# Kernel optimization log

Measured on AMD Instinct MI355X. Metric: run time of the kernel, lower is better.

The kernel has to match this reference:

```python
import jax, jax.numpy as jnp
import numpy as np

N, M, FEAT, POS, D, MSG, NCLS = 64, 32, 256, 6, 262, 128, 7


def setup_inputs() -> dict:
    key = jax.random.key(0)
    ks = jax.random.split(key, 12)
    s = 0.05
    p = lambda k, shape: jax.random.normal(k, shape, jnp.float32) * s
    return {
        "nodes_feature": jax.random.normal(ks[0], (N, M, FEAT), jnp.float32),
        "pos": jax.random.normal(ks[1], (N, M, POS), jnp.float32),
        "num_rec": jax.random.randint(ks[2], (N,), 1, M + 1),
        "link_w1": p(ks[3], (D, 2 * D)),
        "link_b1": jnp.zeros((D,), jnp.float32),
        "link_w2": p(ks[4], (D,)),
        "link_b2": jnp.zeros((), jnp.float32),
        "msg_w": p(ks[5], (MSG, D)),
        "msg_b": jnp.zeros((MSG,), jnp.float32),
        "gru_w_ih": p(ks[6], (3 * D, MSG)),
        "gru_w_hh": p(ks[7], (3 * D, D)),
        "gru_b_ih": jnp.zeros((3 * D,), jnp.float32),
        "gru_b_hh": jnp.zeros((3 * D,), jnp.float32),
        "ro_w1": p(ks[8], (MSG, D)),
        "ro_b1": jnp.zeros((MSG,), jnp.float32),
        "ro_w2": p(ks[9], (NCLS, MSG)),
        "ro_b2": jnp.zeros((NCLS,), jnp.float32),
    }


def reference(nodes_feature, pos, num_rec, link_w1, link_b1, link_w2, link_b2,
              msg_w, msg_b, gru_w_ih, gru_w_hh, gru_b_ih, gru_b_hh,
              ro_w1, ro_b1, ro_w2, ro_b2):
    # node_feat = [resnet_feat, pos]  -> (N, M, 262)
    nf = jnp.concatenate([nodes_feature, pos], axis=-1)
    n, m, d = nf.shape
    valid = jnp.arange(m)[None, :] < num_rec[:, None]          # (N, M)
    pair = valid[:, :, None] & valid[:, None, :]               # (N, M, M)

    # edge_feat[b,:,i,j] = concat(nf[b,i], nf[b,j]); zero for invalid pairs
    ef = jnp.concatenate([
        jnp.broadcast_to(nf[:, :, None, :], (n, m, m, d)),
        jnp.broadcast_to(nf[:, None, :, :], (n, m, m, d)),
    ], axis=-1) * pair[..., None].astype(nf.dtype)             # (N, M, M, 2D)

    # 1x1 convs == per-pair MLP
    hlink = jax.nn.relu(jnp.einsum('bnwc,dc->bnwd', ef, link_w1) + link_b1)
    attmat = jax.nn.sigmoid(jnp.einsum('bnwd,d->bnw', hlink, link_w2) + link_b2)

    # messages are only summed over valid sender nodes w
    att_m = attmat * valid[:, None, :].astype(attmat.dtype)    # (N, M, M)

    def gru_step(x, h):
        # PyTorch GRU cell: gates order (r, z, n)
        gx = x @ gru_w_ih.T + gru_b_ih
        gh = h @ gru_w_hh.T + gru_b_hh
        xr, xz, xn = jnp.split(gx, 3, axis=-1)
        hr, hz, hn = jnp.split(gh, 3, axis=-1)
        r = jax.nn.sigmoid(xr + hr)
        z = jax.nn.sigmoid(xz + hz)
        c = jnp.tanh(xn + r * hn)
        return (1.0 - z) * c + z * h

    vmask = valid[..., None].astype(nf.dtype)
    h_state = nf                                               # pass 0 input state
    for _ in range(2):                                         # two message-passing rounds
        msg = h_state @ msg_w.T + msg_b                        # (N, M, 128)
        m_v = jnp.einsum('bnw,bwk->bnk', att_m, msg)           # attention-weighted sum
        h_state = gru_step(m_v, h_state) * vmask               # invalid nodes stay zero

    pred = (jax.nn.relu(h_state @ ro_w1.T + ro_b1) @ ro_w2.T + ro_b2) * vmask
    return pred, attmat
```

## Files before the change

### kernel.cpp

```cpp
#include <hip/hip_runtime.h>
#include <math.h>

#define N_G   64
#define M_N   32
#define FEAT  256
#define POSD  6
#define D     262
#define MSG   128
#define NCLS  7

#define KA_S  424
#define KHW   288
#define KFULL 416
#define PSTR  320

#define S_PROJ (528*288)
#define S_MSG  (128*288)
#define S_RZ   (544*416)
#define S_XN   (272*128)
#define S_HN   (272*288)
#define S_RO   (128*288)
#define S_RO2  (16*128)

#define O_WPROJ 0u
#define O_WMSG  76032u
#define O_WRZ   94464u
#define O_WXN   207616u
#define O_WHN   225024u
#define O_WRO   264192u
#define O_WRO2  282624u
#define O_GB    283648u

typedef __attribute__((ext_vector_type(8))) short short8;
typedef __attribute__((ext_vector_type(4))) short short4v;
typedef __attribute__((ext_vector_type(4))) float floatx4;

#define MFMA __builtin_amdgcn_mfma_f32_16x16x32_bf16

__device__ __forceinline__ short f2bf(float f) {
    union { float f; unsigned u; } v; v.f = f;
    unsigned r = v.u + 0x7FFF + ((v.u >> 16) & 1);
    return (short)(r >> 16);
}
__device__ __forceinline__ float bf2f(short s) {
    union { float f; unsigned u; } v;
    v.u = ((unsigned)(unsigned short)s) << 16;
    return v.f;
}
__device__ __forceinline__ float sigf(float x) { return 1.f / (1.f + expf(-x)); }

__global__ void prep_kernel(const float* __restrict__ w1, const float* __restrict__ msg_w,
                            const float* __restrict__ w_ih, const float* __restrict__ w_hh,
                            const float* __restrict__ ro_w1, const float* __restrict__ ro_w2,
                            const float* __restrict__ b_ih, const float* __restrict__ b_hh,
                            float* __restrict__ ws)
{
    short* wproj = (short*)(ws + O_WPROJ);
    short* wmsg  = (short*)(ws + O_WMSG);
    short* wrz   = (short*)(ws + O_WRZ);
    short* wxn   = (short*)(ws + O_WXN);
    short* whn   = (short*)(ws + O_WHN);
    short* wro   = (short*)(ws + O_WRO);
    short* wro2  = (short*)(ws + O_WRO2);
    float* gb    = ws + O_GB;
    const int TOT_S = S_PROJ + S_MSG + S_RZ + S_XN + S_HN + S_RO + S_RO2;
    const int TOTAL = TOT_S + 1088;
    for (int i = blockIdx.x * blockDim.x + threadIdx.x; i < TOTAL;
         i += gridDim.x * blockDim.x) {
        int idx = i;
        if (idx < S_PROJ) {
            int n = idx / 288, k = idx % 288;
            float v = 0.f;
            if (k < D && n < 524)
                v = (n < D) ? w1[n * 524 + k] : w1[(n - D) * 524 + D + k];
            wproj[idx] = f2bf(v);
            continue;
        }
        idx -= S_PROJ;
        if (idx < S_MSG) {
            int n = idx / 288, k = idx % 288;
            wmsg[idx] = f2bf(k < D ? msg_w[n * D + k] : 0.f);
            continue;
        }
        idx -= S_MSG;
        if (idx < S_RZ) {
            int g = idx / 416, k = idx % 416;
            int gi = (g < 272) ? 0 : 1;
            int d = g - gi * 272;
            float v = 0.f;
            if (d < D) {
                int row = gi * D + d;
                if (k < 128)            v = w_ih[row * MSG + k];
                else if (k < 128 + D)   v = w_hh[row * D + (k - 128)];
            }
            wrz[idx] = f2bf(v);
            continue;
        }
        idx -= S_RZ;
        if (idx < S_XN) {
            int d = idx / 128, k = idx % 128;
            wxn[idx] = f2bf(d < D ? w_ih[(2 * D + d) * MSG + k] : 0.f);
            continue;
        }
        idx -= S_XN;
        if (idx < S_HN) {
            int d = idx / 288, k = idx % 288;
            whn[idx] = f2bf((d < D && k < D) ? w_hh[(2 * D + d) * D + k] : 0.f);
            continue;
        }
        idx -= S_HN;
        if (idx < S_RO) {
            int n = idx / 288, k = idx % 288;
            wro[idx] = f2bf(k < D ? ro_w1[n * D + k] : 0.f);
            continue;
        }
        idx -= S_RO;
        if (idx < S_RO2) {
            int n = idx / 128, k = idx % 128;
            wro2[idx] = f2bf(n < NCLS ? ro_w2[n * MSG + k] : 0.f);
            continue;
        }
        idx -= S_RO2;
        {
            int seg = idx / 272, d = idx % 272;
            float v = 0.f;
            if (d < D) {
                if (seg == 0)      v = b_ih[d] + b_hh[d];
                else if (seg == 1) v = b_ih[D + d] + b_hh[D + d];
                else if (seg == 2) v = b_ih[2 * D + d];
                else               v = b_hh[2 * D + d];
            }
            gb[idx] = v;
        }
    }
}

__global__ __launch_bounds__(512, 2) void fused_kernel(
    const float* __restrict__ nodes, const float* __restrict__ pos,
    const int* __restrict__ nrec_g,
    const float* __restrict__ b1g, const float* __restrict__ w2g,
    const float* __restrict__ b2g, const float* __restrict__ msg_bg,
    const float* __restrict__ ro_b1g, const float* __restrict__ ro_b2g,
    const float* __restrict__ ws,
    float* __restrict__ att_out, float* __restrict__ pred)
{
    const short* Wproj = (const short*)(ws + O_WPROJ);
    const short* Wmsg  = (const short*)(ws + O_WMSG);
    const short* Wrz   = (const short*)(ws + O_WRZ);
    const short* Wxn   = (const short*)(ws + O_WXN);
    const short* Whn   = (const short*)(ws + O_WHN);
    const short* Wro   = (const short*)(ws + O_WRO);
    const short* Wro2  = (const short*)(ws + O_WRO2);
    const float* gb    = ws + O_GB;

    __shared__ __align__(16) short bufA[32 * KA_S];
    __shared__ __align__(16) short bufB[32 * KA_S];
    __shared__ __align__(16) short paL[32 * PSTR];
    __shared__ __align__(16) short pbL[32 * PSTR];
    __shared__ __align__(16) short attL[32 * 40];
    __shared__ __align__(16) short msgT[128 * 40];
    __shared__ __align__(16) short hidL[32 * 136];
    __shared__ __align__(16) float b1L[PSTR], w2L[PSTR];

    const int b = blockIdx.x;
    const int tid = threadIdx.x;
    const int wave = tid >> 6, lane = tid & 63;
    const int quad = lane >> 4, lrow = lane & 15;
    const int nr = nrec_g[b];

    for (int idx = tid; idx < 32 * 64; idx += 512) {
        int w = idx >> 6, c4 = idx & 63;
        floatx4 v = *(const floatx4*)(nodes + ((size_t)(b * 32 + w)) * FEAT + c4 * 4);
        short4v s; s[0] = f2bf(v[0]); s[1] = f2bf(v[1]); s[2] = f2bf(v[2]); s[3] = f2bf(v[3]);
        *(short4v*)(bufA + w * KA_S + 128 + c4 * 4) = s;
    }
    for (int idx = tid; idx < 32 * POSD; idx += 512) {
        int w = idx / POSD, c = idx % POSD;
        bufA[w * KA_S + 128 + FEAT + c] = f2bf(pos[((size_t)(b * 32 + w)) * POSD + c]);
    }
    for (int idx = tid; idx < 32 * 34; idx += 512) {
        int w = idx / 34, c = idx % 34;
        bufA[w * KA_S + 390 + c] = 0;
        bufB[w * KA_S + 390 + c] = 0;
    }
    for (int idx = tid; idx < 32 * (PSTR - D); idx += 512) {
        int w = idx / (PSTR - D), c = idx % (PSTR - D);
        paL[w * PSTR + D + c] = 0;
        pbL[w * PSTR + D + c] = 0;
    }
    for (int d = tid; d < PSTR; d += 512) {
        b1L[d] = (d < D) ? b1g[d] : 0.f;
        w2L[d] = (d < D) ? w2g[d] : 0.f;
    }
    __syncthreads();

    for (int s = wave; s < 33; s += 8) {
        floatx4 acc0 = {}, acc1 = {};
        const short* bw = Wproj + (s * 16 + lrow) * KHW + quad * 8;
        const short* ap = bufA + lrow * KA_S + 128 + quad * 8;
        for (int kk = 0; kk < 9; ++kk) {
            short8 a0 = *(const short8*)(ap + kk * 32);
            short8 a1 = *(const short8*)(ap + 16 * KA_S + kk * 32);
            short8 bv = *(const short8*)(bw + kk * 32);
            acc0 = MFMA(a0, bv, acc0, 0, 0, 0);
            acc1 = MFMA(a1, bv, acc1, 0, 0, 0);
        }
        int col = s * 16 + lrow;
#pragma unroll
        for (int rr = 0; rr < 4; ++rr) {
            int r0 = quad * 4 + rr;
            if (col < D) {
                paL[r0 * PSTR + col] = f2bf(acc0[rr]);
                paL[(r0 + 16) * PSTR + col] = f2bf(acc1[rr]);
            } else if (col < 2 * D) {
                pbL[r0 * PSTR + (col - D)] = f2bf(acc0[rr]);
                pbL[(r0 + 16) * PSTR + (col - D)] = f2bf(acc1[rr]);
            }
        }
    }
    __syncthreads();

    {
        const int grp = tid >> 4;
        const int c16 = tid & 15;
        const float b2v = b2g[0];
        float pav[5][4], b1v[5][4], w2v[5][4];
#pragma unroll
        for (int k = 0; k < 5; ++k) {
            int dbase = c16 * 4 + 64 * k;
            short4v p = *(const short4v*)(paL + grp * PSTR + dbase);
            floatx4 bb = *(const floatx4*)(b1L + dbase);
            floatx4 ww = *(const floatx4*)(w2L + dbase);
#pragma unroll
            for (int e = 0; e < 4; ++e) {
                pav[k][e] = bf2f(p[e]); b1v[k][e] = bb[e]; w2v[k][e] = ww[e];
            }
        }
        float p0 = 0.f;
#pragma unroll
        for (int k = 0; k < 5; ++k)
#pragma unroll
            for (int e = 0; e < 4; ++e)
                p0 += fmaxf(b1v[k][e], 0.f) * w2v[k][e];
        p0 += __shfl_down(p0, 8, 16); p0 += __shfl_down(p0, 4, 16);
        p0 += __shfl_down(p0, 2, 16); p0 += __shfl_down(p0, 1, 16);
        float c0 = sigf(p0 + b2v);
        const bool vi = grp < nr;
        for (int j = 0; j < 32; ++j) {
            float a;
            if (j < nr && vi) {
                const short* pb = pbL + j * PSTR + c16 * 4;
                float s = 0.f;
#pragma unroll
                for (int k = 0; k < 5; ++k) {
                    short4v q = *(const short4v*)(pb + 64 * k);
#pragma unroll
                    for (int e = 0; e < 4; ++e) {
                        float v = pav[k][e] + bf2f(q[e]) + b1v[k][e];
                        s += fmaxf(v, 0.f) * w2v[k][e];
                    }
                }
                s += __shfl_down(s, 8, 16); s += __shfl_down(s, 4, 16);
                s += __shfl_down(s, 2, 16); s += __shfl_down(s, 1, 16);
                a = sigf(s + b2v);
            } else {
                a = c0;
            }
            if (c16 == 0) {
                att_out[((size_t)(b * 32 + grp)) * 32 + j] = a;
                attL[grp * 40 + j] = f2bf((j < nr) ? a : 0.f);
            }
        }
    }
    __syncthreads();

    for (int rnd = 0; rnd < 2; ++rnd) {
        short* src = rnd ? bufB : bufA;
        short* dst = rnd ? bufA : bufB;

        {
            int s = wave;
            floatx4 acc0 = {}, acc1 = {};
            const short* bw = Wmsg + (s * 16 + lrow) * KHW + quad * 8;
            const short* ap = src + lrow * KA_S + 128 + quad * 8;
            for (int kk = 0; kk < 9; ++kk) {
                short8 a0 = *(const short8*)(ap + kk * 32);
                short8 a1 = *(const short8*)(ap + 16 * KA_S + kk * 32);
                short8 bv = *(const short8*)(bw + kk * 32);
                acc0 = MFMA(a0, bv, acc0, 0, 0, 0);
                acc1 = MFMA(a1, bv, acc1, 0, 0, 0);
            }
            int col = s * 16 + lrow;
            float bias = msg_bg[col];
#pragma unroll
            for (int rr = 0; rr < 4; ++rr) {
                msgT[col * 40 + quad * 4 + rr] = f2bf(acc0[rr] + bias);
                msgT[col * 40 + 16 + quad * 4 + rr] = f2bf(acc1[rr] + bias);
            }
        }
        __syncthreads();

        {
            int mi = wave & 1, ng = wave >> 1;
            short8 afrag = *(const short8*)(attL + (mi * 16 + lrow) * 40 + quad * 8);
            floatx4 acc0 = {}, acc1 = {};
            short8 bf0 = *(const short8*)(msgT + (ng * 32 + lrow) * 40 + quad * 8);
            short8 bf1 = *(const short8*)(msgT + (ng * 32 + 16 + lrow) * 40 + quad * 8);
            acc0 = MFMA(afrag, bf0, acc0, 0, 0, 0);
            acc1 = MFMA(afrag, bf1, acc1, 0, 0, 0);
#pragma unroll
            for (int rr = 0; rr < 4; ++rr) {
                int m = mi * 16 + quad * 4 + rr;
                src[m * KA_S + ng * 32 + lrow] = f2bf(acc0[rr]);
                src[m * KA_S + ng * 32 + 16 + lrow] = f2bf(acc1[rr]);
            }
        }
        __syncthreads();

        for (int s = wave; s < 17; s += 8) {
            floatx4 aR0 = {}, aR1 = {}, aZ0 = {}, aZ1 = {};
            floatx4 aN0 = {}, aN1 = {}, aH0 = {}, aH1 = {};
            const short* ap  = src + lrow * KA_S + quad * 8;
            const short* bpr = Wrz + (s * 16 + lrow) * KFULL + quad * 8;
            const short* bpz = Wrz + (272 + s * 16 + lrow) * KFULL + quad * 8;
            const short* bpx = Wxn + (s * 16 + lrow) * 128 + quad * 8;
            const short* bph = Whn + (s * 16 + lrow) * KHW + quad * 8;
            for (int kk = 0; kk < 13; ++kk) {
                short8 a0 = *(const short8*)(ap + kk * 32);
                short8 a1 = *(const short8*)(ap + 16 * KA_S + kk * 32);
                short8 br = *(const short8*)(bpr + kk * 32);
                short8 bz = *(const short8*)(bpz + kk * 32);
                aR0 = MFMA(a0, br, aR0, 0, 0, 0);
                aR1 = MFMA(a1, br, aR1, 0, 0, 0);
                aZ0 = MFMA(a0, bz, aZ0, 0, 0, 0);
                aZ1 = MFMA(a1, bz, aZ1, 0, 0, 0);
                if (kk < 4) {
                    short8 bx = *(const short8*)(bpx + kk * 32);
                    aN0 = MFMA(a0, bx, aN0, 0, 0, 0);
                    aN1 = MFMA(a1, bx, aN1, 0, 0, 0);
                } else {
                    short8 bh = *(const short8*)(bph + (kk - 4) * 32);
                    aH0 = MFMA(a0, bh, aH0, 0, 0, 0);
                    aH1 = MFMA(a1, bh, aH1, 0, 0, 0);
                }
            }
            int d = s * 16 + lrow;
            if (d < D) {
                float bgr = gb[d], bgz = gb[272 + d];
                float bxv = gb[544 + d], bhv = gb[816 + d];
#pragma unroll
                for (int i = 0; i < 2; ++i) {
                    floatx4 vR = i ? aR1 : aR0, vZ = i ? aZ1 : aZ0;
                    floatx4 vN = i ? aN1 : aN0, vH = i ? aH1 : aH0;
#pragma unroll
                    for (int rr = 0; rr < 4; ++rr) {
                        int m = i * 16 + quad * 4 + rr;
                        float rg = sigf(vR[rr] + bgr);
                        float zg = sigf(vZ[rr] + bgz);
                        float cg = tanhf(vN[rr] + bxv + rg * (vH[rr] + bhv));
                        float hold = bf2f(src[m * KA_S + 128 + d]);
                        float hv = (1.f - zg) * cg + zg * hold;
                        if (m >= nr) hv = 0.f;
                        dst[m * KA_S + 128 + d] = f2bf(hv);
                    }
                }
            }
        }
        __syncthreads();
    }

    {
        int s = wave;
        floatx4 acc0 = {}, acc1 = {};
        const short* bw = Wro + (s * 16 + lrow) * KHW + quad * 8;
        const short* ap = bufA + lrow * KA_S + 128 + quad * 8;
        for (int kk = 0; kk < 9; ++kk) {
            short8 a0 = *(const short8*)(ap + kk * 32);
            short8 a1 = *(const short8*)(ap + 16 * KA_S + kk * 32);
            short8 bv = *(const short8*)(bw + kk * 32);
            acc0 = MFMA(a0, bv, acc0, 0, 0, 0);
            acc1 = MFMA(a1, bv, acc1, 0, 0, 0);
        }
        int col = s * 16 + lrow;
        float bias = ro_b1g[col];
#pragma unroll
        for (int rr = 0; rr < 4; ++rr) {
            hidL[(quad * 4 + rr) * 136 + col] = f2bf(fmaxf(acc0[rr] + bias, 0.f));
            hidL[(16 + quad * 4 + rr) * 136 + col] = f2bf(fmaxf(acc1[rr] + bias, 0.f));
        }
    }
    __syncthreads();

    if (wave == 0) {
        floatx4 acc0 = {}, acc1 = {};
        const short* ap = hidL + lrow * 136 + quad * 8;
        const short* bw = Wro2 + lrow * 128 + quad * 8;
        for (int kk = 0; kk < 4; ++kk) {
            short8 a0 = *(const short8*)(ap + kk * 32);
            short8 a1 = *(const short8*)(ap + 16 * 136 + kk * 32);
            short8 bv = *(const short8*)(bw + kk * 32);
            acc0 = MFMA(a0, bv, acc0, 0, 0, 0);
            acc1 = MFMA(a1, bv, acc1, 0, 0, 0);
        }
        int q = lrow;
        if (q < NCLS) {
            float bias = ro_b2g[q];
#pragma unroll
            for (int i = 0; i < 2; ++i) {
#pragma unroll
                for (int rr = 0; rr < 4; ++rr) {
                    int m = i * 16 + quad * 4 + rr;
                    float v = (i ? acc1[rr] : acc0[rr]) + bias;
                    if (m >= nr) v = 0.f;
                    pred[((size_t)(b * 32 + m)) * NCLS + q] = v;
                }
            }
        }
    }
}

extern "C" void kernel_launch(void* const* d_in, const int* in_sizes, int n_in,
                              void* d_out, int out_size, void* d_ws, size_t ws_size,
                              hipStream_t stream)
{
    const float* nodes = (const float*)d_in[0];
    const float* pos   = (const float*)d_in[1];
    const int*   nrec  = (const int*)d_in[2];
    const float* w1    = (const float*)d_in[3];
    const float* b1    = (const float*)d_in[4];
    const float* w2    = (const float*)d_in[5];
    const float* b2    = (const float*)d_in[6];
    const float* msg_w = (const float*)d_in[7];
    const float* msg_b = (const float*)d_in[8];
    const float* w_ih  = (const float*)d_in[9];
    const float* w_hh  = (const float*)d_in[10];
    const float* b_ih  = (const float*)d_in[11];
    const float* b_hh  = (const float*)d_in[12];
    const float* ro_w1 = (const float*)d_in[13];
    const float* ro_b1 = (const float*)d_in[14];
    const float* ro_w2 = (const float*)d_in[15];
    const float* ro_b2 = (const float*)d_in[16];
    float* ws   = (float*)d_ws;
    float* pred = (float*)d_out;
    float* attout = pred + (size_t)N_G * M_N * NCLS;

    prep_kernel<<<256, 256, 0, stream>>>(w1, msg_w, w_ih, w_hh, ro_w1, ro_w2,
                                         b_ih, b_hh, ws);
    fused_kernel<<<N_G, 512, 0, stream>>>(nodes, pos, nrec, b1, w2, b2, msg_b,
                                          ro_b1, ro_b2, ws, attout, pred);
}
```

Before: 160.4 us.

## Double block size to 1024 threads and repartition work across 16 waves

Raises the per-graph block from 512 to 1024 threads and splits each stage's work across 16 waves instead of 8: message, aggregation and readout GEMMs now give each wave a single 16-row tile, and the pairwise attention loop splits the j range between two thread groups. The link bias b1 is folded into the projected pa values once, and the inner attention loop now uses 8-wide bf16 loads over a padded stride of 384. With only 64 blocks on the GPU, the goal is more parallelism per graph to cut latency. The cost is fewer registers per thread under the 1024-thread bound and more barrier participants. Some loops, such as the GRU stage with 17 slabs, leave waves idle.

```diff
diff --git a/kernel.cpp b/kernel.cpp
--- a/kernel.cpp
+++ b/kernel.cpp
@@ -9,10 +9,11 @@
 #define MSG   128
 #define NCLS  7
 
+#define NT    1024
 #define KA_S  424
 #define KHW   288
 #define KFULL 416
-#define PSTR  320
+#define PSTR  384
 
 #define S_PROJ (528*288)
 #define S_MSG  (128*288)
@@ -135,7 +136,7 @@
     }
 }
 
-__global__ __launch_bounds__(512, 2) void fused_kernel(
+__global__ __launch_bounds__(NT, 4) void fused_kernel(
     const float* __restrict__ nodes, const float* __restrict__ pos,
     const int* __restrict__ nrec_g,
     const float* __restrict__ b1g, const float* __restrict__ w2g,
@@ -168,33 +169,33 @@
     const int quad = lane >> 4, lrow = lane & 15;
     const int nr = nrec_g[b];
 
-    for (int idx = tid; idx < 32 * 64; idx += 512) {
+    for (int idx = tid; idx < 32 * 64; idx += NT) {
         int w = idx >> 6, c4 = idx & 63;
         floatx4 v = *(const floatx4*)(nodes + ((size_t)(b * 32 + w)) * FEAT + c4 * 4);
         short4v s; s[0] = f2bf(v[0]); s[1] = f2bf(v[1]); s[2] = f2bf(v[2]); s[3] = f2bf(v[3]);
         *(short4v*)(bufA + w * KA_S + 128 + c4 * 4) = s;
     }
-    for (int idx = tid; idx < 32 * POSD; idx += 512) {
+    for (int idx = tid; idx < 32 * POSD; idx += NT) {
         int w = idx / POSD, c = idx % POSD;
         bufA[w * KA_S + 128 + FEAT + c] = f2bf(pos[((size_t)(b * 32 + w)) * POSD + c]);
     }
-    for (int idx = tid; idx < 32 * 34; idx += 512) {
+    for (int idx = tid; idx < 32 * 34; idx += NT) {
         int w = idx / 34, c = idx % 34;
         bufA[w * KA_S + 390 + c] = 0;
         bufB[w * KA_S + 390 + c] = 0;
     }
-    for (int idx = tid; idx < 32 * (PSTR - D); idx += 512) {
+    for (int idx = tid; idx < 32 * (PSTR - D); idx += NT) {
         int w = idx / (PSTR - D), c = idx % (PSTR - D);
         paL[w * PSTR + D + c] = 0;
         pbL[w * PSTR + D + c] = 0;
     }
-    for (int d = tid; d < PSTR; d += 512) {
+    for (int d = tid; d < PSTR; d += NT) {
         b1L[d] = (d < D) ? b1g[d] : 0.f;
         w2L[d] = (d < D) ? w2g[d] : 0.f;
     }
     __syncthreads();
 
-    for (int s = wave; s < 33; s += 8) {
+    for (int s = wave; s < 33; s += 16) {
         floatx4 acc0 = {}, acc1 = {};
         const short* bw = Wproj + (s * 16 + lrow) * KHW + quad * 8;
         const short* ap = bufA + lrow * KA_S + 128 + quad * 8;
@@ -210,8 +211,9 @@
         for (int rr = 0; rr < 4; ++rr) {
             int r0 = quad * 4 + rr;
             if (col < D) {
-                paL[r0 * PSTR + col] = f2bf(acc0[rr]);
-                paL[(r0 + 16) * PSTR + col] = f2bf(acc1[rr]);
+                float bb = b1L[col];
+                paL[r0 * PSTR + col] = f2bf(acc0[rr] + bb);
+                paL[(r0 + 16) * PSTR + col] = f2bf(acc1[rr] + bb);
             } else if (col < 2 * D) {
                 pbL[r0 * PSTR + (col - D)] = f2bf(acc0[rr]);
                 pbL[(r0 + 16) * PSTR + (col - D)] = f2bf(acc1[rr]);
@@ -222,43 +224,51 @@
 
     {
         const int grp = tid >> 4;
+        const int i = grp >> 1;
+        const int jb = (grp & 1) * 16;
         const int c16 = tid & 15;
         const float b2v = b2g[0];
-        float pav[5][4], b1v[5][4], w2v[5][4];
-#pragma unroll
-        for (int k = 0; k < 5; ++k) {
-            int dbase = c16 * 4 + 64 * k;
-            short4v p = *(const short4v*)(paL + grp * PSTR + dbase);
-            floatx4 bb = *(const floatx4*)(b1L + dbase);
-            floatx4 ww = *(const floatx4*)(w2L + dbase);
+        float pav[3][8], w2v[3][8];
+#pragma unroll
+        for (int k = 0; k < 3; ++k) {
+            int dbase = c16 * 8 + 128 * k;
+            short8 p = *(const short8*)(paL + i * PSTR + dbase);
+            floatx4 wa = *(const floatx4*)(w2L + dbase);
+            floatx4 wb = *(const floatx4*)(w2L + dbase + 4);
 #pragma unroll
             for (int e = 0; e < 4; ++e) {
-                pav[k][e] = bf2f(p[e]); b1v[k][e] = bb[e]; w2v[k][e] = ww[e];
+                pav[k][e] = bf2f(p[e]); pav[k][4 + e] = bf2f(p[4 + e]);
+                w2v[k][e] = wa[e]; w2v[k][4 + e] = wb[e];
             }
         }
         float p0 = 0.f;
 #pragma unroll
-        for (int k = 0; k < 5; ++k)
-#pragma unroll
-            for (int e = 0; e < 4; ++e)
-                p0 += fmaxf(b1v[k][e], 0.f) * w2v[k][e];
+        for (int k = 0; k < 3; ++k) {
+            int dbase = c16 * 8 + 128 * k;
+            floatx4 ba = *(const floatx4*)(b1L + dbase);
+            floatx4 bb = *(const floatx4*)(b1L + dbase + 4);
+#pragma unroll
+            for (int e = 0; e < 4; ++e) {
+                p0 += fmaxf(ba[e], 0.f) * w2v[k][e];
+                p0 += fmaxf(bb[e], 0.f) * w2v[k][4 + e];
+            }
+        }
         p0 += __shfl_down(p0, 8, 16); p0 += __shfl_down(p0, 4, 16);
         p0 += __shfl_down(p0, 2, 16); p0 += __shfl_down(p0, 1, 16);
         float c0 = sigf(p0 + b2v);
-        const bool vi = grp < nr;
-        for (int j = 0; j < 32; ++j) {
+        const bool vi = i < nr;
+        for (int jj = 0; jj < 16; ++jj) {
+            int j = jb + jj;
             float a;
-            if (j < nr && vi) {
-                const short* pb = pbL + j * PSTR + c16 * 4;
+            if (vi && j < nr) {
+                const short* pb = pbL + j * PSTR + c16 * 8;
                 float s = 0.f;
 #pragma unroll
-                for (int k = 0; k < 5; ++k) {
-                    short4v q = *(const short4v*)(pb + 64 * k);
-#pragma unroll
-                    for (int e = 0; e < 4; ++e) {
-                        float v = pav[k][e] + bf2f(q[e]) + b1v[k][e];
-                        s += fmaxf(v, 0.f) * w2v[k][e];
-                    }
+                for (int k = 0; k < 3; ++k) {
+                    short8 q = *(const short8*)(pb + 128 * k);
+#pragma unroll
+                    for (int e = 0; e < 8; ++e)
+                        s += fmaxf(pav[k][e] + bf2f(q[e]), 0.f) * w2v[k][e];
                 }
                 s += __shfl_down(s, 8, 16); s += __shfl_down(s, 4, 16);
                 s += __shfl_down(s, 2, 16); s += __shfl_down(s, 1, 16);
@@ -267,8 +277,8 @@
                 a = c0;
             }
             if (c16 == 0) {
-                att_out[((size_t)(b * 32 + grp)) * 32 + j] = a;
-                attL[grp * 40 + j] = f2bf((j < nr) ? a : 0.f);
+                att_out[((size_t)(b * 32 + i)) * 32 + j] = a;
+                attL[i * 40 + j] = f2bf((j < nr) ? a : 0.f);
             }
         }
     }
@@ -279,45 +289,38 @@
         short* dst = rnd ? bufA : bufB;
 
         {
-            int s = wave;
-            floatx4 acc0 = {}, acc1 = {};
+            int s = wave >> 1, mi = wave & 1;
+            floatx4 acc = {};
             const short* bw = Wmsg + (s * 16 + lrow) * KHW + quad * 8;
-            const short* ap = src + lrow * KA_S + 128 + quad * 8;
+            const short* ap = src + (mi * 16 + lrow) * KA_S + 128 + quad * 8;
             for (int kk = 0; kk < 9; ++kk) {
                 short8 a0 = *(const short8*)(ap + kk * 32);
-                short8 a1 = *(const short8*)(ap + 16 * KA_S + kk * 32);
                 short8 bv = *(const short8*)(bw + kk * 32);
-                acc0 = MFMA(a0, bv, acc0, 0, 0, 0);
-                acc1 = MFMA(a1, bv, acc1, 0, 0, 0);
+                acc = MFMA(a0, bv, acc, 0, 0, 0);
             }
             int col = s * 16 + lrow;
             float bias = msg_bg[col];
 #pragma unroll
-            for (int rr = 0; rr < 4; ++rr) {
-                msgT[col * 40 + quad * 4 + rr] = f2bf(acc0[rr] + bias);
-                msgT[col * 40 + 16 + quad * 4 + rr] = f2bf(acc1[rr] + bias);
-            }
+            for (int rr = 0; rr < 4; ++rr)
+                msgT[col * 40 + mi * 16 + quad * 4 + rr] = f2bf(acc[rr] + bias);
         }
         __syncthreads();
 
         {
             int mi = wave & 1, ng = wave >> 1;
             short8 afrag = *(const short8*)(attL + (mi * 16 + lrow) * 40 + quad * 8);
-            floatx4 acc0 = {}, acc1 = {};
-            short8 bf0 = *(const short8*)(msgT + (ng * 32 + lrow) * 40 + quad * 8);
-            short8 bf1 = *(const short8*)(msgT + (ng * 32 + 16 + lrow) * 40 + quad * 8);
-            acc0 = MFMA(afrag, bf0, acc0, 0, 0, 0);
-            acc1 = MFMA(afrag, bf1, acc1, 0, 0, 0);
+            short8 bfrag = *(const short8*)(msgT + (ng * 16 + lrow) * 40 + quad * 8);
+            floatx4 acc = {};
+            acc = MFMA(afrag, bfrag, acc, 0, 0, 0);
 #pragma unroll
             for (int rr = 0; rr < 4; ++rr) {
                 int m = mi * 16 + quad * 4 + rr;
-                src[m * KA_S + ng * 32 + lrow] = f2bf(acc0[rr]);
-                src[m * KA_S + ng * 32 + 16 + lrow] = f2bf(acc1[rr]);
+                src[m * KA_S + ng * 16 + lrow] = f2bf(acc[rr]);
             }
         }
         __syncthreads();
 
-        for (int s = wave; s < 17; s += 8) {
+        for (int s = wave; s < 17; s += 16) {
             floatx4 aR0 = {}, aR1 = {}, aZ0 = {}, aZ1 = {};
             floatx4 aN0 = {}, aN1 = {}, aH0 = {}, aH1 = {};
             const short* ap  = src + lrow * KA_S + quad * 8;
@@ -370,24 +373,20 @@
     }
 
     {
-        int s = wave;
-        floatx4 acc0 = {}, acc1 = {};
+        int s = wave >> 1, mi = wave & 1;
+        floatx4 acc = {};
         const short* bw = Wro + (s * 16 + lrow) * KHW + quad * 8;
-        const short* ap = bufA + lrow * KA_S + 128 + quad * 8;
+        const short* ap = bufA + (mi * 16 + lrow) * KA_S + 128 + quad * 8;
         for (int kk = 0; kk < 9; ++kk) {
             short8 a0 = *(const short8*)(ap + kk * 32);
-            short8 a1 = *(const short8*)(ap + 16 * KA_S + kk * 32);
             short8 bv = *(const short8*)(bw + kk * 32);
-            acc0 = MFMA(a0, bv, acc0, 0, 0, 0);
-            acc1 = MFMA(a1, bv, acc1, 0, 0, 0);
+            acc = MFMA(a0, bv, acc, 0, 0, 0);
         }
         int col = s * 16 + lrow;
         float bias = ro_b1g[col];
 #pragma unroll
-        for (int rr = 0; rr < 4; ++rr) {
-            hidL[(quad * 4 + rr) * 136 + col] = f2bf(fmaxf(acc0[rr] + bias, 0.f));
-            hidL[(16 + quad * 4 + rr) * 136 + col] = f2bf(fmaxf(acc1[rr] + bias, 0.f));
-        }
+        for (int rr = 0; rr < 4; ++rr)
+            hidL[(mi * 16 + quad * 4 + rr) * 136 + col] = f2bf(fmaxf(acc[rr] + bias, 0.f));
     }
     __syncthreads();
 
@@ -446,6 +445,6 @@
 
     prep_kernel<<<256, 256, 0, stream>>>(w1, msg_w, w_ih, w_hh, ro_w1, ro_w2,
                                          b_ih, b_hh, ws);
-    fused_kernel<<<N_G, 512, 0, stream>>>(nodes, pos, nrec, b1, w2, b2, msg_b,
-                                          ro_b1, ro_b2, ws, attout, pred);
+    fused_kernel<<<N_G, NT, 0, stream>>>(nodes, pos, nrec, b1, w2, b2, msg_b,
+                                         ro_b1, ro_b2, ws, attout, pred);
 }
```

Measured after the change: 195.2 us. 1.22x slower.

## Restructure attention pair loop, fold link bias into projection, use fast transcendentals

Applied to the files above, without the earlier changes.

The pairwise attention stage is remapped so each lane computes one (i,j) pair for two rows directly over the full feature dimension. This replaces the earlier scheme of 16-lane groups looping serially over j with shuffle reductions. The link bias b1 is folded into the projected pa values, and the constant attention value for invalid pairs is now computed once in the prep kernel. Sigmoid and tanh switch to hardware exp2/rcp intrinsics, and the shared-memory row stride shrinks to 266. The risks are LDS bank conflicts from the odd stride and slightly lower precision in the activations.

```diff
diff --git a/kernel.cpp b/kernel.cpp
--- a/kernel.cpp
+++ b/kernel.cpp
@@ -12,7 +12,7 @@
 #define KA_S  424
 #define KHW   288
 #define KFULL 416
-#define PSTR  320
+#define PSTR  266
 
 #define S_PROJ (528*288)
 #define S_MSG  (128*288)
@@ -47,12 +47,21 @@
     v.u = ((unsigned)(unsigned short)s) << 16;
     return v.f;
 }
-__device__ __forceinline__ float sigf(float x) { return 1.f / (1.f + expf(-x)); }
+__device__ __forceinline__ float sigf(float x) {
+    float e = __builtin_amdgcn_exp2f(x * -1.442695041f);
+    return __builtin_amdgcn_rcpf(1.f + e);
+}
+__device__ __forceinline__ float tanhf_fast(float x) {
+    float e = __builtin_amdgcn_exp2f(x * 2.885390082f);
+    return 1.f - 2.f * __builtin_amdgcn_rcpf(e + 1.f);
+}
 
 __global__ void prep_kernel(const float* __restrict__ w1, const float* __restrict__ msg_w,
                             const float* __restrict__ w_ih, const float* __restrict__ w_hh,
                             const float* __restrict__ ro_w1, const float* __restrict__ ro_w2,
                             const float* __restrict__ b_ih, const float* __restrict__ b_hh,
+                            const float* __restrict__ b1g, const float* __restrict__ w2g,
+                            const float* __restrict__ b2g,
                             float* __restrict__ ws)
 {
     short* wproj = (short*)(ws + O_WPROJ);
@@ -64,7 +73,7 @@
     short* wro2  = (short*)(ws + O_WRO2);
     float* gb    = ws + O_GB;
     const int TOT_S = S_PROJ + S_MSG + S_RZ + S_XN + S_HN + S_RO + S_RO2;
-    const int TOTAL = TOT_S + 1088;
+    const int TOTAL = TOT_S + 1089;
     for (int i = blockIdx.x * blockDim.x + threadIdx.x; i < TOTAL;
          i += gridDim.x * blockDim.x) {
         int idx = i;
@@ -121,7 +130,7 @@
             continue;
         }
         idx -= S_RO2;
-        {
+        if (idx < 1088) {
             int seg = idx / 272, d = idx % 272;
             float v = 0.f;
             if (d < D) {
@@ -131,6 +140,13 @@
                 else               v = b_hh[2 * D + d];
             }
             gb[idx] = v;
+            continue;
+        }
+        {
+            float s = 0.f;
+            for (int d = 0; d < D; ++d)
+                s += fmaxf(b1g[d], 0.f) * w2g[d];
+            gb[1088] = sigf(s + b2g[0]);
         }
     }
 }
@@ -160,7 +176,7 @@
     __shared__ __align__(16) short attL[32 * 40];
     __shared__ __align__(16) short msgT[128 * 40];
     __shared__ __align__(16) short hidL[32 * 136];
-    __shared__ __align__(16) float b1L[PSTR], w2L[PSTR];
+    __shared__ __align__(16) float b1L[PSTR + 6], w2L[PSTR + 6];
 
     const int b = blockIdx.x;
     const int tid = threadIdx.x;
@@ -188,7 +204,7 @@
         paL[w * PSTR + D + c] = 0;
         pbL[w * PSTR + D + c] = 0;
     }
-    for (int d = tid; d < PSTR; d += 512) {
+    for (int d = tid; d < PSTR + 6; d += 512) {
         b1L[d] = (d < D) ? b1g[d] : 0.f;
         w2L[d] = (d < D) ? w2g[d] : 0.f;
     }
@@ -210,8 +226,9 @@
         for (int rr = 0; rr < 4; ++rr) {
             int r0 = quad * 4 + rr;
             if (col < D) {
-                paL[r0 * PSTR + col] = f2bf(acc0[rr]);
-                paL[(r0 + 16) * PSTR + col] = f2bf(acc1[rr]);
+                float bb = b1L[col];
+                paL[r0 * PSTR + col] = f2bf(acc0[rr] + bb);
+                paL[(r0 + 16) * PSTR + col] = f2bf(acc1[rr] + bb);
             } else if (col < 2 * D) {
                 pbL[r0 * PSTR + (col - D)] = f2bf(acc0[rr]);
                 pbL[(r0 + 16) * PSTR + (col - D)] = f2bf(acc1[rr]);
@@ -221,56 +238,37 @@
     __syncthreads();
 
     {
-        const int grp = tid >> 4;
-        const int c16 = tid & 15;
+        const float c0 = gb[1088];
         const float b2v = b2g[0];
-        float pav[5][4], b1v[5][4], w2v[5][4];
-#pragma unroll
-        for (int k = 0; k < 5; ++k) {
-            int dbase = c16 * 4 + 64 * k;
-            short4v p = *(const short4v*)(paL + grp * PSTR + dbase);
-            floatx4 bb = *(const floatx4*)(b1L + dbase);
-            floatx4 ww = *(const floatx4*)(w2L + dbase);
-#pragma unroll
-            for (int e = 0; e < 4; ++e) {
-                pav[k][e] = bf2f(p[e]); b1v[k][e] = bb[e]; w2v[k][e] = ww[e];
-            }
-        }
-        float p0 = 0.f;
-#pragma unroll
-        for (int k = 0; k < 5; ++k)
-#pragma unroll
-            for (int e = 0; e < 4; ++e)
-                p0 += fmaxf(b1v[k][e], 0.f) * w2v[k][e];
-        p0 += __shfl_down(p0, 8, 16); p0 += __shfl_down(p0, 4, 16);
-        p0 += __shfl_down(p0, 2, 16); p0 += __shfl_down(p0, 1, 16);
-        float c0 = sigf(p0 + b2v);
-        const bool vi = grp < nr;
-        for (int j = 0; j < 32; ++j) {
-            float a;
-            if (j < nr && vi) {
-                const short* pb = pbL + j * PSTR + c16 * 4;
-                float s = 0.f;
-#pragma unroll
-                for (int k = 0; k < 5; ++k) {
-                    short4v q = *(const short4v*)(pb + 64 * k);
-#pragma unroll
-                    for (int e = 0; e < 4; ++e) {
-                        float v = pav[k][e] + bf2f(q[e]) + b1v[k][e];
-                        s += fmaxf(v, 0.f) * w2v[k][e];
-                    }
-                }
-                s += __shfl_down(s, 8, 16); s += __shfl_down(s, 4, 16);
-                s += __shfl_down(s, 2, 16); s += __shfl_down(s, 1, 16);
-                a = sigf(s + b2v);
-            } else {
-                a = c0;
-            }
-            if (c16 == 0) {
-                att_out[((size_t)(b * 32 + grp)) * 32 + j] = a;
-                attL[grp * 40 + j] = f2bf((j < nr) ? a : 0.f);
-            }
-        }
+        const int jj = lane & 31;
+        const int i0 = 2 * wave + (lane >> 5);
+        const int i1 = i0 + 16;
+        const short* pa0 = paL + i0 * PSTR;
+        const short* pa1 = paL + i1 * PSTR;
+        const short* pbr = pbL + jj * PSTR;
+        float s0 = 0.f, s1 = 0.f;
+        for (int c = 0; c < 33; ++c) {
+            int d = c * 8;
+            short8 qa0 = *(const short8*)(pa0 + d);
+            short8 qa1 = *(const short8*)(pa1 + d);
+            short8 qb  = *(const short8*)(pbr + d);
+            floatx4 wlo = *(const floatx4*)(w2L + d);
+            floatx4 whi = *(const floatx4*)(w2L + d + 4);
+#pragma unroll
+            for (int e = 0; e < 8; ++e) {
+                float w = (e < 4) ? wlo[e] : whi[e - 4];
+                float pbv = bf2f(qb[e]);
+                s0 += fmaxf(bf2f(qa0[e]) + pbv, 0.f) * w;
+                s1 += fmaxf(bf2f(qa1[e]) + pbv, 0.f) * w;
+            }
+        }
+        const bool vj = jj < nr;
+        float a0 = (vj && i0 < nr) ? sigf(s0 + b2v) : c0;
+        float a1 = (vj && i1 < nr) ? sigf(s1 + b2v) : c0;
+        att_out[((size_t)(b * 32 + i0)) * 32 + jj] = a0;
+        att_out[((size_t)(b * 32 + i1)) * 32 + jj] = a1;
+        attL[i0 * 40 + jj] = f2bf(vj ? a0 : 0.f);
+        attL[i1 * 40 + jj] = f2bf(vj ? a1 : 0.f);
     }
     __syncthreads();
 
@@ -357,7 +355,7 @@
                         int m = i * 16 + quad * 4 + rr;
                         float rg = sigf(vR[rr] + bgr);
                         float zg = sigf(vZ[rr] + bgz);
-                        float cg = tanhf(vN[rr] + bxv + rg * (vH[rr] + bhv));
+                        float cg = tanhf_fast(vN[rr] + bxv + rg * (vH[rr] + bhv));
                         float hold = bf2f(src[m * KA_S + 128 + d]);
                         float hv = (1.f - zg) * cg + zg * hold;
                         if (m >= nr) hv = 0.f;
@@ -445,7 +443,7 @@
     float* attout = pred + (size_t)N_G * M_N * NCLS;
 
     prep_kernel<<<256, 256, 0, stream>>>(w1, msg_w, w_ih, w_hh, ro_w1, ro_w2,
-                                         b_ih, b_hh, ws);
+                                         b_ih, b_hh, b1, w2, b2, ws);
     fused_kernel<<<N_G, 512, 0, stream>>>(nodes, pos, nrec, b1, w2, b2, msg_b,
                                           ro_b1, ro_b2, ws, attout, pred);
 }
```

Measured after the change: 169.1 us. +5.4%, slower.
